# Optimization experiments

Measured on AMD Instinct MI355X. Metric: run time of the kernel, lower is better.

Reference implementation:

```python
import jax, jax.numpy as jnp
import numpy as np

EPS_SCALE = 1e-4

def setup_inputs() -> dict:
    key = jax.random.key(0)
    B, D, K = 4096, 64, 256
    x = jax.random.normal(key, (B, D, K), dtype=jnp.float32)
    return {"x": x}

def reference(x):
    # x: [B, D, K]  (batch, cluster_dim, num_clusters) -- training path
    B, D, K = x.shape
    mu = jnp.mean(x, axis=0, keepdims=True)              # [1, D, K]
    xc = jnp.transpose(x - mu, (2, 1, 0))                # [K, D, B]
    cov = jnp.einsum('kdb,keb->kde', xc, xc) / (B - 1)   # [K, D, D]
    eps = EPS_SCALE * jnp.eye(D, dtype=x.dtype)
    L = jnp.linalg.cholesky(cov + eps)                   # [K, D, D]
    Z = jax.scipy.linalg.solve_triangular(L, xc, lower=True)  # [K, D, B]
    return jnp.transpose(Z, (2, 1, 0))                   # [B, D, K]
```

## Files before the change

kernel.cpp:

```cpp
#include <hip/hip_runtime.h>
#include <math.h>

#define Bn 4096
#define Dn 64
#define Kn 256
#define DKn 16384
#define SLAB ((size_t)262144)

typedef __attribute__((ext_vector_type(8))) short bf16x8;
typedef __attribute__((ext_vector_type(4))) float f32x4;
typedef unsigned short u16;
typedef unsigned int u32;

__device__ __forceinline__ float bf2f(u16 u) {
  return __uint_as_float(((u32)u) << 16);
}
__device__ __forceinline__ u16 f2bf(float f) {
  u32 x = __float_as_uint(f);
  u32 r = x + 0x7fffu + ((x >> 16) & 1u);
  return (u16)(r >> 16);
}

__global__ __launch_bounds__(256) void k1_transpose(
    const float* __restrict__ x, u16* __restrict__ xh) {
  __shared__ __align__(16) u16 tile[64][72];
  const int b0 = blockIdx.x * 8;
  const int k0 = blockIdx.y * 64;
  const int t = threadIdx.x;
  const int kq = t & 15, dsub = t >> 4;
  const int kr = t >> 3, dq = t & 7;

  for (int bb = 0; bb < 8; ++bb) {
    const int b = b0 + bb;
#pragma unroll
    for (int i = 0; i < 4; ++i) {
      const int d = dsub + 16 * i;
      const float4 v = *(const float4*)&x[(size_t)b * DKn + (size_t)d * Kn + k0 + 4 * kq];
      tile[4 * kq + 0][d] = f2bf(v.x);
      tile[4 * kq + 1][d] = f2bf(v.y);
      tile[4 * kq + 2][d] = f2bf(v.z);
      tile[4 * kq + 3][d] = f2bf(v.w);
    }
    __syncthreads();
#pragma unroll
    for (int it = 0; it < 2; ++it) {
      const int k = kr + 32 * it;
      const uint4 wv = *(const uint4*)&tile[k][8 * dq];
      *(uint4*)&xh[(size_t)(k0 + k) * SLAB + (size_t)b * 64 + 8 * dq] = wv;
    }
    __syncthreads();
  }
}

__global__ __launch_bounds__(256) void k2_cov(
    const u16* __restrict__ xh, float* __restrict__ covp, float* __restrict__ Sp) {
  __shared__ __align__(16) u16 tile[64][136];
  __shared__ float sred[32][64];
  const int part = blockIdx.x;
  const int k = blockIdx.y;
  const int t = threadIdx.x;
  const int w = t >> 6, l = t & 63;
  const int r16 = l & 15, g = l >> 4;
  const int dw = t & 7, bq = t >> 3;
  const u16* pk = xh + (size_t)k * SLAB;

  f32x4 hh[10];
#pragma unroll
  for (int p = 0; p < 10; ++p) hh[p] = (f32x4){0.f, 0.f, 0.f, 0.f};
  float sums[8];
#pragma unroll
  for (int jj = 0; jj < 8; ++jj) sums[jj] = 0.f;

  for (int sub = 0; sub < 8; ++sub) {
    const int bbase = part * 1024 + sub * 128;
    __syncthreads();
#pragma unroll
    for (int i = 0; i < 4; ++i) {
      const int b = bq * 4 + i;
      const uint4 v = *(const uint4*)&pk[(size_t)(bbase + b) * 64 + dw * 8];
      const u16* pv = (const u16*)&v;
#pragma unroll
      for (int jj = 0; jj < 8; ++jj) {
        const u16 h = pv[jj];
        sums[jj] += bf2f(h);
        tile[dw * 8 + jj][b] = h;
      }
    }
    __syncthreads();
    bf16x8 fr[4];
#pragma unroll
    for (int m = 0; m < 4; ++m)
      fr[m] = *(const bf16x8*)&tile[16 * m + r16][32 * w + 8 * g];
#pragma unroll
    for (int m = 0; m < 4; ++m)
#pragma unroll
      for (int n = m; n < 4; ++n) {
        const int p = (m * (7 - m)) / 2 + n;
        hh[p] = __builtin_amdgcn_mfma_f32_16x16x32_bf16(fr[m], fr[n], hh[p], 0, 0, 0);
      }
  }
  float* cp = covp + ((size_t)k * 16 + part * 4 + w) * 2560;
#pragma unroll
  for (int p = 0; p < 10; ++p)
#pragma unroll
    for (int r = 0; r < 4; ++r)
      cp[p * 256 + (g * 4 + r) * 16 + r16] = hh[p][r];
#pragma unroll
  for (int jj = 0; jj < 8; ++jj) sred[bq][dw * 8 + jj] = sums[jj];
  __syncthreads();
  if (t < 64) {
    float s = 0.f;
#pragma unroll
    for (int q = 0; q < 32; ++q) s += sred[q][t];
    Sp[((size_t)k * 4 + part) * 64 + t] = s;
  }
}

__global__ __launch_bounds__(256) void k3_chol(
    const float* __restrict__ covp, const float* __restrict__ Sp,
    u16* __restrict__ wt, u16* __restrict__ vout) {
  __shared__ float a[64][65];
  __shared__ float mus[64];
  __shared__ float colv[64];
  __shared__ float diag;
  const int k = blockIdx.x;
  const int tid = threadIdx.x;
  if (tid < 64) {
    float s = 0.f;
#pragma unroll
    for (int q = 0; q < 4; ++q) s += Sp[((size_t)k * 4 + q) * 64 + tid];
    mus[tid] = s * (1.f / 4096.f);
  }
  __syncthreads();
  const float* cp = covp + (size_t)k * 16 * 2560;
  for (int idx = tid; idx < 4096; idx += 256) {
    const int i = idx >> 6, j = idx & 63;
    const int i16 = i >> 4, j16 = j >> 4, r = i & 15, c = j & 15;
    int p, off;
    if (i16 <= j16) { p = (i16 * (7 - i16)) / 2 + j16; off = r * 16 + c; }
    else            { p = (j16 * (7 - j16)) / 2 + i16; off = c * 16 + r; }
    float s = 0.f;
#pragma unroll
    for (int q = 0; q < 16; ++q) s += cp[q * 2560 + p * 256 + off];
    float cv = (s - 4096.f * mus[i] * mus[j]) * (1.f / 4095.f);
    if (i == j) cv += 1e-4f;
    a[i][j] = cv;
  }
  __syncthreads();
  for (int j = 0; j < 64; ++j) {
    if (tid == j) diag = sqrtf(a[j][j]);
    __syncthreads();
    const float ljj = diag;
    float lij = 0.f;
    if (tid == j) a[j][j] = ljj;
    if (tid < 64 && tid > j) {
      lij = a[tid][j] / ljj;
      a[tid][j] = lij;
      colv[tid] = lij;
    }
    __syncthreads();
    if (tid < 64 && tid > j)
      for (int e = j + 1; e <= tid; ++e) a[tid][e] -= lij * colv[e];
    __syncthreads();
  }
  float wv[64];
  if (tid < 64) {
#pragma unroll
    for (int i = 0; i < 64; ++i) {
      float s2 = (i == tid) ? 1.f : 0.f;
#pragma unroll
      for (int j = 0; j < i; ++j) s2 -= a[i][j] * wv[j];
      wv[i] = (i >= tid) ? s2 / a[i][i] : 0.f;
    }
  }
  __syncthreads();
  if (tid < 64) {
#pragma unroll
    for (int i = 0; i < 64; ++i) a[i][tid] = wv[i];
  }
  __syncthreads();
  if (tid < 64) {
    float v = 0.f;
#pragma unroll
    for (int e = 0; e < 64; ++e) v += a[tid][e] * mus[e];
    vout[(size_t)k * 64 + tid] = f2bf(v);
  }
#pragma unroll
  for (int it = 0; it < 8; ++it) {
    const int idx = it * 256 + tid;
    const int dd = idx >> 5, ep = idx & 31;
    const u32 pk2 = (u32)f2bf(a[dd][2 * ep]) | ((u32)f2bf(a[dd][2 * ep + 1]) << 16);
    *(u32*)&wt[(size_t)k * 4096 + 2 * idx] = pk2;
  }
}

union SMemU {
  u16 xstage[2][8][16][64];
  u16 zls[16][17][68];
};

__global__ __launch_bounds__(256) void k45_solve(
    const u16* __restrict__ xh, const u16* __restrict__ wt,
    const u16* __restrict__ vin, float* __restrict__ out) {
  __shared__ SMemU sm;
  __shared__ __align__(16) u16 vsh[32][72];
  const int b0 = blockIdx.x * 16;
  const int kc0 = blockIdx.y * 32;
  const int t = threadIdx.x;
  const int w = t >> 6, l = t & 63;
  const int r16 = l & 15, g = l >> 4;

  *(uint4*)&vsh[t >> 3][8 * (t & 7)] = *(const uint4*)&vin[(size_t)kc0 * 64 + t * 8];

  uint4 sv[4];
#pragma unroll
  for (int i = 0; i < 4; ++i) {
    const int idx = i * 256 + t;
    const int kk = idx >> 7, b = (idx >> 3) & 15, dc = idx & 7;
    sv[i] = *(const uint4*)&xh[(size_t)(kc0 + kk) * SLAB + (size_t)(b0 + b) * 64 + dc * 8];
  }
#pragma unroll
  for (int i = 0; i < 4; ++i) {
    const int idx = i * 256 + t;
    const int kk = idx >> 7, b = (idx >> 3) & 15, dc = idx & 7;
    *(uint4*)&sm.xstage[0][kk][b][(dc ^ (b & 7)) * 8] = sv[i];
  }
  __syncthreads();

  bf16x8 a0, a1, an0, an1;
  {
    const u16* wk = wt + (size_t)kc0 * 4096 + (16 * w + r16) * 64 + 8 * g;
    a0 = *(const bf16x8*)(wk);
    a1 = *(const bf16x8*)(wk + 32);
  }

  u32 zr[64];

#pragma unroll
  for (int rnd = 0; rnd < 4; ++rnd) {
    if (rnd < 3) {
#pragma unroll
      for (int i = 0; i < 4; ++i) {
        const int idx = i * 256 + t;
        const int kk = idx >> 7, b = (idx >> 3) & 15, dc = idx & 7;
        sv[i] = *(const uint4*)&xh[(size_t)(kc0 + (rnd + 1) * 8 + kk) * SLAB +
                                   (size_t)(b0 + b) * 64 + dc * 8];
      }
    }
#pragma unroll
    for (int kk = 0; kk < 8; ++kk) {
      const int kidx = rnd * 8 + kk;
      if (kidx < 31) {
        const u16* wk = wt + (size_t)(kc0 + kidx + 1) * 4096 + (16 * w + r16) * 64 + 8 * g;
        an0 = *(const bf16x8*)(wk);
        an1 = *(const bf16x8*)(wk + 32);
      }
      const bf16x8 bf0 = *(const bf16x8*)&sm.xstage[rnd & 1][kk][r16][(g ^ (r16 & 7)) * 8];
      const bf16x8 bf1 = *(const bf16x8*)&sm.xstage[rnd & 1][kk][r16][((4 + g) ^ (r16 & 7)) * 8];
      f32x4 acc = (f32x4){0.f, 0.f, 0.f, 0.f};
      acc = __builtin_amdgcn_mfma_f32_16x16x32_bf16(a0, bf0, acc, 0, 0, 0);
      acc = __builtin_amdgcn_mfma_f32_16x16x32_bf16(a1, bf1, acc, 0, 0, 0);
      zr[2 * kidx] = (u32)f2bf(acc[0]) | ((u32)f2bf(acc[1]) << 16);
      zr[2 * kidx + 1] = (u32)f2bf(acc[2]) | ((u32)f2bf(acc[3]) << 16);
      a0 = an0; a1 = an1;
    }
    if (rnd < 3) {
#pragma unroll
      for (int i = 0; i < 4; ++i) {
        const int idx = i * 256 + t;
        const int kk = idx >> 7, b = (idx >> 3) & 15, dc = idx & 7;
        *(uint4*)&sm.xstage[(rnd + 1) & 1][kk][b][(dc ^ (b & 7)) * 8] = sv[i];
      }
      __syncthreads();
    }
  }
  __syncthreads();

  const int d0 = 16 * w + 4 * g;
  const int d0s = d0 ^ ((r16 & 3) << 2);
#pragma unroll
  for (int h = 0; h < 2; ++h) {
#pragma unroll
    for (int kkl = 0; kkl < 16; ++kkl) {
      const int kk = h * 16 + kkl;
      uint2 st;
      st.x = zr[2 * kk];
      st.y = zr[2 * kk + 1];
      *(uint2*)&sm.zls[r16][kkl][d0s] = st;
    }
    __syncthreads();
#pragma unroll
    for (int it = 0; it < 16; ++it) {
      const int c = w * 256 + it * 16 + (l >> 2);
      const int kc = l & 3;
      const int b = c >> 6, d = c & 63;
      const int ds = d ^ ((b & 3) << 2);
      float4 ov;
#pragma unroll
      for (int j = 0; j < 4; ++j) {
        const int kl = 4 * kc + j;
        ((float*)&ov)[j] = bf2f(sm.zls[b][kl][ds]) - bf2f(vsh[h * 16 + kl][d]);
      }
      *(float4*)&out[(size_t)(b0 + b) * DKn + (size_t)d * Kn + kc0 + h * 16 + 4 * kc] = ov;
    }
    __syncthreads();
  }
}

extern "C" void kernel_launch(void* const* d_in, const int* in_sizes, int n_in,
                              void* d_out, int out_size, void* d_ws, size_t ws_size,
                              hipStream_t stream) {
  (void)in_sizes; (void)n_in; (void)out_size;
  const float* x = (const float*)d_in[0];
  float* out = (float*)d_out;
  char* ws = (char*)d_ws;
  const size_t XH_B = 134217728;
  const size_t CP_B = 41943040;
  const size_t SP_B = 262144;
  const size_t WT_B = 2097152;
  const size_t V_B  = 32768;
  if (ws_size < XH_B + CP_B + SP_B + WT_B + V_B) return;
  u16* xh = (u16*)ws;
  float* covp = (float*)(ws + XH_B);
  float* Sp = (float*)(ws + XH_B + CP_B);
  u16* wtb = (u16*)(ws + XH_B + CP_B + SP_B);
  u16* vb  = (u16*)(ws + XH_B + CP_B + SP_B + WT_B);

  k1_transpose<<<dim3(512, 4), 256, 0, stream>>>(x, xh);
  k2_cov<<<dim3(4, 256), 256, 0, stream>>>(xh, covp, Sp);
  k3_chol<<<dim3(256), 256, 0, stream>>>(covp, Sp, wtb, vb);
  k45_solve<<<dim3(256, 8), 256, 0, stream>>>(xh, wtb, vb, out);
}
```

Baseline: 401.4 us.

## Rework transpose, cov staging and deepen weight prefetch in solve kernel

The transpose kernel now stages fp32 values in a padded shared tile and converts to bf16 on the write side, cutting the per-element 16-bit shared stores. The covariance kernel loads two batch rows per lane and writes packed 32-bit pairs into the shared tile, with a reshaped reduction buffer for the column sums. The solve kernel prefetches weight fragments four clusters ahead in a ring of registers instead of one ahead, to hide global-load latency. This adds register pressure and changes the bank-conflict pattern in several shared-memory accesses.

```diff
diff --git a/kernel.cpp b/kernel.cpp
--- a/kernel.cpp
+++ b/kernel.cpp
@@ -23,12 +23,12 @@
 
 __global__ __launch_bounds__(256) void k1_transpose(
     const float* __restrict__ x, u16* __restrict__ xh) {
-  __shared__ __align__(16) u16 tile[64][72];
+  __shared__ float tf[64][65];
   const int b0 = blockIdx.x * 8;
   const int k0 = blockIdx.y * 64;
   const int t = threadIdx.x;
   const int kq = t & 15, dsub = t >> 4;
-  const int kr = t >> 3, dq = t & 7;
+  const int dq = t & 7, kr = t >> 3;
 
   for (int bb = 0; bb < 8; ++bb) {
     const int b = b0 + bb;
@@ -36,17 +36,24 @@
     for (int i = 0; i < 4; ++i) {
       const int d = dsub + 16 * i;
       const float4 v = *(const float4*)&x[(size_t)b * DKn + (size_t)d * Kn + k0 + 4 * kq];
-      tile[4 * kq + 0][d] = f2bf(v.x);
-      tile[4 * kq + 1][d] = f2bf(v.y);
-      tile[4 * kq + 2][d] = f2bf(v.z);
-      tile[4 * kq + 3][d] = f2bf(v.w);
+      tf[4 * kq + 0][d] = v.x;
+      tf[4 * kq + 1][d] = v.y;
+      tf[4 * kq + 2][d] = v.z;
+      tf[4 * kq + 3][d] = v.w;
     }
     __syncthreads();
 #pragma unroll
     for (int it = 0; it < 2; ++it) {
       const int k = kr + 32 * it;
-      const uint4 wv = *(const uint4*)&tile[k][8 * dq];
-      *(uint4*)&xh[(size_t)(k0 + k) * SLAB + (size_t)b * 64 + 8 * dq] = wv;
+      u32 pk[4];
+#pragma unroll
+      for (int j = 0; j < 4; ++j) {
+        const float f0 = tf[k][8 * dq + 2 * j];
+        const float f1 = tf[k][8 * dq + 2 * j + 1];
+        pk[j] = (u32)f2bf(f0) | ((u32)f2bf(f1) << 16);
+      }
+      *(uint4*)&xh[(size_t)(k0 + k) * SLAB + (size_t)b * 64 + 8 * dq] =
+          make_uint4(pk[0], pk[1], pk[2], pk[3]);
     }
     __syncthreads();
   }
@@ -55,35 +62,36 @@
 __global__ __launch_bounds__(256) void k2_cov(
     const u16* __restrict__ xh, float* __restrict__ covp, float* __restrict__ Sp) {
   __shared__ __align__(16) u16 tile[64][136];
-  __shared__ float sred[32][64];
+  __shared__ float sred[64][65];
   const int part = blockIdx.x;
   const int k = blockIdx.y;
   const int t = threadIdx.x;
   const int w = t >> 6, l = t & 63;
   const int r16 = l & 15, g = l >> 4;
-  const int dw = t & 7, bq = t >> 3;
   const u16* pk = xh + (size_t)k * SLAB;
 
   f32x4 hh[10];
 #pragma unroll
   for (int p = 0; p < 10; ++p) hh[p] = (f32x4){0.f, 0.f, 0.f, 0.f};
-  float sums[8];
-#pragma unroll
-  for (int jj = 0; jj < 8; ++jj) sums[jj] = 0.f;
+  float dsums[16];
+#pragma unroll
+  for (int q = 0; q < 16; ++q) dsums[q] = 0.f;
 
   for (int sub = 0; sub < 8; ++sub) {
     const int bbase = part * 1024 + sub * 128;
     __syncthreads();
 #pragma unroll
-    for (int i = 0; i < 4; ++i) {
-      const int b = bq * 4 + i;
-      const uint4 v = *(const uint4*)&pk[(size_t)(bbase + b) * 64 + dw * 8];
-      const u16* pv = (const u16*)&v;
+    for (int iter = 0; iter < 2; ++iter) {
+      const int dwc = w + 4 * iter;
+      const uint4 v0 = *(const uint4*)&pk[(size_t)(bbase + 2 * l) * 64 + dwc * 8];
+      const uint4 v1 = *(const uint4*)&pk[(size_t)(bbase + 2 * l + 1) * 64 + dwc * 8];
+      const u16* p0 = (const u16*)&v0;
+      const u16* p1 = (const u16*)&v1;
 #pragma unroll
       for (int jj = 0; jj < 8; ++jj) {
-        const u16 h = pv[jj];
-        sums[jj] += bf2f(h);
-        tile[dw * 8 + jj][b] = h;
+        const u16 h0 = p0[jj], h1 = p1[jj];
+        dsums[iter * 8 + jj] += bf2f(h0) + bf2f(h1);
+        *(u32*)&tile[8 * dwc + jj][2 * l] = (u32)h0 | ((u32)h1 << 16);
       }
     }
     __syncthreads();
@@ -106,12 +114,15 @@
     for (int r = 0; r < 4; ++r)
       cp[p * 256 + (g * 4 + r) * 16 + r16] = hh[p][r];
 #pragma unroll
-  for (int jj = 0; jj < 8; ++jj) sred[bq][dw * 8 + jj] = sums[jj];
+  for (int iter = 0; iter < 2; ++iter)
+#pragma unroll
+    for (int jj = 0; jj < 8; ++jj)
+      sred[8 * (w + 4 * iter) + jj][l] = dsums[iter * 8 + jj];
   __syncthreads();
   if (t < 64) {
     float s = 0.f;
 #pragma unroll
-    for (int q = 0; q < 32; ++q) s += sred[q][t];
+    for (int q = 0; q < 64; ++q) s += sred[t][q];
     Sp[((size_t)k * 4 + part) * 64 + t] = s;
   }
 }
@@ -225,14 +236,15 @@
     const int kk = idx >> 7, b = (idx >> 3) & 15, dc = idx & 7;
     *(uint4*)&sm.xstage[0][kk][b][(dc ^ (b & 7)) * 8] = sv[i];
   }
-  __syncthreads();
-
-  bf16x8 a0, a1, an0, an1;
-  {
-    const u16* wk = wt + (size_t)kc0 * 4096 + (16 * w + r16) * 64 + 8 * g;
-    a0 = *(const bf16x8*)(wk);
-    a1 = *(const bf16x8*)(wk + 32);
-  }
+
+  bf16x8 af0[4], af1[4];
+#pragma unroll
+  for (int p = 0; p < 4; ++p) {
+    const u16* wk = wt + (size_t)(kc0 + p) * 4096 + (16 * w + r16) * 64 + 8 * g;
+    af0[p] = *(const bf16x8*)(wk);
+    af1[p] = *(const bf16x8*)(wk + 32);
+  }
+  __syncthreads();
 
   u32 zr[64];
 
@@ -250,10 +262,12 @@
 #pragma unroll
     for (int kk = 0; kk < 8; ++kk) {
       const int kidx = rnd * 8 + kk;
-      if (kidx < 31) {
-        const u16* wk = wt + (size_t)(kc0 + kidx + 1) * 4096 + (16 * w + r16) * 64 + 8 * g;
-        an0 = *(const bf16x8*)(wk);
-        an1 = *(const bf16x8*)(wk + 32);
+      const bf16x8 a0 = af0[kidx & 3];
+      const bf16x8 a1 = af1[kidx & 3];
+      if (kidx + 4 < 32) {
+        const u16* wk = wt + (size_t)(kc0 + kidx + 4) * 4096 + (16 * w + r16) * 64 + 8 * g;
+        af0[kidx & 3] = *(const bf16x8*)(wk);
+        af1[kidx & 3] = *(const bf16x8*)(wk + 32);
       }
       const bf16x8 bf0 = *(const bf16x8*)&sm.xstage[rnd & 1][kk][r16][(g ^ (r16 & 7)) * 8];
       const bf16x8 bf1 = *(const bf16x8*)&sm.xstage[rnd & 1][kk][r16][((4 + g) ^ (r16 & 7)) * 8];
@@ -262,7 +276,6 @@
       acc = __builtin_amdgcn_mfma_f32_16x16x32_bf16(a1, bf1, acc, 0, 0, 0);
       zr[2 * kidx] = (u32)f2bf(acc[0]) | ((u32)f2bf(acc[1]) << 16);
       zr[2 * kidx + 1] = (u32)f2bf(acc[2]) | ((u32)f2bf(acc[3]) << 16);
-      a0 = an0; a1 = an1;
     }
     if (rnd < 3) {
 #pragma unroll
```

After: 376.4 us. -6.2%, faster.
